# Kernel optimization log

Measured on AMD Instinct MI355X. Metric: run time of the kernel, lower is better.

Reference implementation:

```python
import jax, jax.numpy as jnp
import numpy as np

RADIUS = 0.2
K = 32
H_RES = 480
W_RES = 640
DIM = 128
EPS = 1e-5  # BatchNorm2d default eps


def setup_inputs() -> dict:
    key = jax.random.key(0)
    k1, k2, k3 = jax.random.split(key, 3)
    B, N = 2, 4096
    xyzp = jax.random.normal(k1, (B, N, 4), jnp.float32)
    features = jax.random.normal(k2, (B, N, DIM), jnp.float32)
    Wm = jax.random.normal(k3, (2 * DIM + 9, DIM), jnp.float32) * 0.05
    b = jnp.zeros((DIM,), jnp.float32)
    gamma = jnp.ones((DIM,), jnp.float32)
    beta = jnp.zeros((DIM,), jnp.float32)
    return {"xyzp": xyzp, "features": features, "Wm": Wm, "b": b, "gamma": gamma, "beta": beta}


def _ball_query(xyz, radius, k):
    # pytorch3d-style ball query: first k point indices (in index order) within radius, pad -1
    B, N, _ = xyz.shape
    d2 = jnp.sum((xyz[:, :, None, :] - xyz[:, None, :, :]) ** 2, axis=-1)  # [B,N,N]
    mask = d2 < radius * radius
    keyv = jnp.where(mask, jnp.arange(N)[None, None, :], N)
    order = jnp.argsort(keyv, axis=-1)[:, :, :k]  # stable sort -> first indices within radius
    count = mask.sum(axis=-1)
    return jnp.where(jnp.arange(k)[None, None, :] < count[:, :, None], order, -1)


def _knn_gather(x, idx):
    # x: [B,N,C], idx: [B,N,K] -> [B,N,K,C]
    B, N, Kk = idx.shape
    flat = idx.reshape(B, N * Kk)
    return jnp.take_along_axis(x, flat[:, :, None], axis=1).reshape(B, N, Kk, x.shape[-1])


def reference(xyzp, features, Wm, b, gamma, beta):
    B, N, _ = xyzp.shape
    # detached xyz with z (time) zeroed, used only for neighbor search
    xyz = jax.lax.stop_gradient(xyzp[..., :3]).at[..., 2].set(0.0)
    idx = _ball_query(xyz, RADIUS, K)
    self_idx = jnp.broadcast_to(jnp.arange(N)[None, :, None], (B, N, K))
    idx = jnp.where(idx == -1, self_idx, idx)

    d = xyzp[:, :, None, :] - _knn_gather(xyzp, idx)  # [B,N,K,4]
    ts = d[..., 2:3]
    ts = jnp.where(ts == 0, jnp.float32(1e-6), ts)
    res = jnp.array([W_RES, H_RES], jnp.float32)
    speed = d[..., :2] / ts * res  # [B,N,K,2]
    mean_speed = jnp.broadcast_to(speed.mean(axis=(1, 2), keepdims=True), speed.shape)
    p = jnp.abs(d[..., 3:4])

    knn_f = _knn_gather(features, idx)  # [B,N,K,DIM]
    f0 = jnp.broadcast_to(features[:, :, None, :], (B, N, K, features.shape[-1]))
    f = jnp.concatenate([f0, knn_f, d, speed, p, mean_speed], axis=-1)  # [B,N,K,2*DIM+9]

    h = f @ Wm + b  # Linear
    # BatchNorm2d in training mode: per-channel stats over (B,N,K)
    mu = h.mean(axis=(0, 1, 2))
    var = h.var(axis=(0, 1, 2))
    h = (h - mu) / jnp.sqrt(var + EPS) * gamma + beta
    h = jax.nn.relu(h)
    return h.max(axis=-2)  # max over K neighbors -> [B,N,DIM]
```

## Files before the change

### kernel.cpp

```cpp
#include <hip/hip_runtime.h>
#include <math.h>

#define NB   2
#define NP   4096
#define KNN  32
#define DIMC 128
#define NROWS (NB*NP)
#define MTOT  (NB*NP*KNN)
#define K2BLOCKS 512
#define MAINBLOCKS 512

static constexpr float R2 = 0.04f;

__global__ __launch_bounds__(256) void k1(const float* __restrict__ feat,
                                          const float* __restrict__ Wm,
                                          float* __restrict__ e,
                                          float* __restrict__ g)
{
    const int t    = threadIdx.x;
    const int lane = t & 63;
    const int wid  = __builtin_amdgcn_readfirstlane(t >> 6);
    const int wgl  = blockIdx.x * 4 + wid;
    const int row0 = (wgl >> 2) * 8;
    const int cg   = wgl & 3;
    const int wbase = (cg >> 1) * 128;
    const int c0    = (cg & 1) * 64;

    const float* __restrict__ fptr = feat + (size_t)row0 * DIMC;
    const float* __restrict__ wptr = Wm + (size_t)wbase * DIMC + c0 + lane;

    float acc[8];
    #pragma unroll
    for (int r = 0; r < 8; ++r) acc[r] = 0.f;

    #pragma unroll 2
    for (int k4 = 0; k4 < 32; ++k4) {
        float bv[4];
        #pragma unroll
        for (int j = 0; j < 4; ++j)
            bv[j] = wptr[(size_t)(k4*4 + j)*DIMC];
        float4 as[8];
        #pragma unroll
        for (int r = 0; r < 8; ++r)
            as[r] = *(const float4*)(fptr + (size_t)r*DIMC + k4*4);
        #pragma unroll
        for (int r = 0; r < 8; ++r) {
            acc[r] = fmaf(as[r].x, bv[0], acc[r]);
            acc[r] = fmaf(as[r].y, bv[1], acc[r]);
            acc[r] = fmaf(as[r].z, bv[2], acc[r]);
            acc[r] = fmaf(as[r].w, bv[3], acc[r]);
        }
    }

    float* dst = (cg >> 1) ? g : e;
    #pragma unroll
    for (int r = 0; r < 8; ++r)
        dst[(size_t)(row0 + r)*DIMC + c0 + lane] = acc[r];
}

__global__ __launch_bounds__(256) void k2(const float* __restrict__ xyzp,
                                          const float* __restrict__ e,
                                          const float* __restrict__ g,
                                          const float* __restrict__ Wm,
                                          const float* __restrict__ bbias,
                                          double* __restrict__ spart,
                                          float* __restrict__ hmaxA,
                                          float* __restrict__ hminA,
                                          float* __restrict__ stpartT)
{
    __shared__ float xy[NP*2];
    __shared__ int   idxrow[16*KNN];
    __shared__ float geo[4][2][KNN][8];
    __shared__ float l1s[8][DIMC];
    __shared__ float l2s[8][DIMC];
    __shared__ float swr[8];

    const int bx  = blockIdx.x;
    const int xcd = bx & 7;
    const int pb  = ((xcd >> 2) << 8) + (bx >> 3)*4 + (xcd & 3);
    const int b   = pb >> 8;
    const int p0  = (pb & 255) * 16;

    const int t    = threadIdx.x;
    const int w    = t >> 6;
    const int lane = t & 63;
    const float* xb = xyzp + (size_t)b*NP*4;

    for (int q = t; q < NP; q += 256) {
        const float4 v = *(const float4*)(xb + (size_t)q*4);
        xy[q*2 + 0] = v.x;
        xy[q*2 + 1] = v.y;
    }
    __syncthreads();

    const int pl0 = p0 + w*4;
    unsigned long long wacc[4] = {0ULL, 0ULL, 0ULL, 0ULL};
    {
#pragma clang fp contract(off)
        float xi[4], yi[4];
        #pragma unroll
        for (int p = 0; p < 4; ++p) { xi[p] = xy[(pl0+p)*2]; yi[p] = xy[(pl0+p)*2+1]; }
        for (int c = 0; c < NP/64; ++c) {
            const float2 q = *(const float2*)(xy + (size_t)(c*64 + lane)*2);
            const bool keep = (lane == c);
            #pragma unroll
            for (int p = 0; p < 4; ++p) {
                const float dx = xi[p] - q.x;
                const float dy = yi[p] - q.y;
                const float dx2 = dx*dx;
                const float dy2 = dy*dy;
                const unsigned long long m = __ballot((dx2 + dy2) < R2);
                if (keep) wacc[p] = m;
            }
        }
    }

    #pragma unroll
    for (int p = 0; p < 4; ++p) {
        unsigned long long wd = wacc[p];
        const int cnt = __popcll(wd);
        int pre = cnt;
        #pragma unroll
        for (int off = 1; off < 64; off <<= 1) {
            const int tv = __shfl_up(pre, off);
            if (lane >= off) pre += tv;
        }
        const int total = __shfl(pre, 63);
        int slot = pre - cnt;
        unsigned long long ww = wd;
        while (ww != 0ULL && slot < KNN) {
            const int bpos = __builtin_ctzll(ww);
            idxrow[(w*4 + p)*KNN + slot] = lane*64 + bpos;
            ww &= ww - 1ULL;
            ++slot;
        }
        const int iself = pl0 + p;
        for (int kk = min(total, KNN) + lane; kk < KNN; kk += 64)
            idxrow[(w*4 + p)*KNN + kk] = iself;
    }

    const int half = lane >> 5;
    const int lq   = lane & 31;
    const int c0   = lq * 4;
    float4 w2r[7];
    #pragma unroll
    for (int r = 0; r < 7; ++r)
        w2r[r] = *(const float4*)(Wm + (size_t)(256 + r)*DIMC + c0);
    const float4 bb4 = *(const float4*)(bbias + c0);

    float s1x=0.f,s1y=0.f,s1z=0.f,s1w=0.f;
    float s2x=0.f,s2y=0.f,s2z=0.f,s2w=0.f;
    float sxacc = 0.f, syacc = 0.f;
    const float* gbb = g + (size_t)b*NP*DIMC + c0;

    for (int rp = 0; rp < 2; ++rp) {
        const int rloc = w*4 + rp*2 + half;
        const int ptl  = p0 + rloc;
        const int j0   = idxrow[rloc*KNN + lq];
        const float4 pj = *(const float4*)(xb + (size_t)j0*4);
        const float4 pi = *(const float4*)(xb + (size_t)ptl*4);
        const float dx = pi.x - pj.x;
        const float dy = pi.y - pj.y;
        const float dz = pi.z - pj.z;
        const float dwv = pi.w - pj.w;
        const float ts  = (dz == 0.f) ? 1e-6f : dz;
        const float rts = __builtin_amdgcn_rcpf(ts);
        const float sxv = dx*rts*640.f;
        const float syv = dy*rts*480.f;
        *(float4*)&geo[w][half][lq][0] = make_float4(dx, dy, dz, dwv);
        *(float4*)&geo[w][half][lq][4] = make_float4(sxv, syv, fabsf(dwv), __int_as_float(j0));
        sxacc += sxv; syacc += syv;
        __builtin_amdgcn_wave_barrier();

        const size_t rowg = (size_t)b*NP + ptl;
        const float4 ee = *(const float4*)(e + rowg*DIMC + c0);
        const float ecx = ee.x + bb4.x, ecy = ee.y + bb4.y;
        const float ecz = ee.z + bb4.z, ecw = ee.w + bb4.w;
        float mxx=-INFINITY,mxy=-INFINITY,mxz=-INFINITY,mxw=-INFINITY;
        float mnx= INFINITY,mny= INFINITY,mnz= INFINITY,mnw= INFINITY;
        #pragma unroll 4
        for (int k = 0; k < KNN; ++k) {
            const float4 g0 = *(const float4*)&geo[w][half][k][0];
            const float4 g1 = *(const float4*)&geo[w][half][k][4];
            const int jj = __float_as_int(g1.w);
            const float4 gg = *(const float4*)(gbb + (size_t)jj*DIMC);

            float h0 = ecx + gg.x;
            h0 = fmaf(g0.x, w2r[0].x, h0); h0 = fmaf(g0.y, w2r[1].x, h0);
            h0 = fmaf(g0.z, w2r[2].x, h0); h0 = fmaf(g0.w, w2r[3].x, h0);
            h0 = fmaf(g1.x, w2r[4].x, h0); h0 = fmaf(g1.y, w2r[5].x, h0);
            h0 = fmaf(g1.z, w2r[6].x, h0);
            mxx = fmaxf(mxx, h0); mnx = fminf(mnx, h0);
            s1x += h0; s2x = fmaf(h0, h0, s2x);

            float h1 = ecy + gg.y;
            h1 = fmaf(g0.x, w2r[0].y, h1); h1 = fmaf(g0.y, w2r[1].y, h1);
            h1 = fmaf(g0.z, w2r[2].y, h1); h1 = fmaf(g0.w, w2r[3].y, h1);
            h1 = fmaf(g1.x, w2r[4].y, h1); h1 = fmaf(g1.y, w2r[5].y, h1);
            h1 = fmaf(g1.z, w2r[6].y, h1);
            mxy = fmaxf(mxy, h1); mny = fminf(mny, h1);
            s1y += h1; s2y = fmaf(h1, h1, s2y);

            float h2 = ecz + gg.z;
            h2 = fmaf(g0.x, w2r[0].z, h2); h2 = fmaf(g0.y, w2r[1].z, h2);
            h2 = fmaf(g0.z, w2r[2].z, h2); h2 = fmaf(g0.w, w2r[3].z, h2);
            h2 = fmaf(g1.x, w2r[4].z, h2); h2 = fmaf(g1.y, w2r[5].z, h2);
            h2 = fmaf(g1.z, w2r[6].z, h2);
            mxz = fmaxf(mxz, h2); mnz = fminf(mnz, h2);
            s1z += h2; s2z = fmaf(h2, h2, s2z);

            float h3 = ecw + gg.w;
            h3 = fmaf(g0.x, w2r[0].w, h3); h3 = fmaf(g0.y, w2r[1].w, h3);
            h3 = fmaf(g0.z, w2r[2].w, h3); h3 = fmaf(g0.w, w2r[3].w, h3);
            h3 = fmaf(g1.x, w2r[4].w, h3); h3 = fmaf(g1.y, w2r[5].w, h3);
            h3 = fmaf(g1.z, w2r[6].w, h3);
            mxw = fmaxf(mxw, h3); mnw = fminf(mnw, h3);
            s1w += h3; s2w = fmaf(h3, h3, s2w);
        }
        *(float4*)(hmaxA + rowg*DIMC + c0) = make_float4(mxx, mxy, mxz, mxw);
        *(float4*)(hminA + rowg*DIMC + c0) = make_float4(mnx, mny, mnz, mnw);
        __builtin_amdgcn_wave_barrier();
    }

    #pragma unroll
    for (int off = 32; off > 0; off >>= 1) {
        sxacc += __shfl_down(sxacc, off);
        syacc += __shfl_down(syacc, off);
    }
    if (lane == 0) { swr[w*2] = sxacc; swr[w*2+1] = syacc; }

    *(float4*)&l1s[w*2 + half][c0] = make_float4(s1x, s1y, s1z, s1w);
    *(float4*)&l2s[w*2 + half][c0] = make_float4(s2x, s2y, s2z, s2w);
    __syncthreads();
    if (t < DIMC) {
        float v = 0.f;
        #pragma unroll
        for (int r = 0; r < 8; ++r) v += l1s[r][t];
        stpartT[(size_t)t*MAINBLOCKS + pb] = v;
    } else {
        const int c = t - DIMC;
        float v = 0.f;
        #pragma unroll
        for (int r = 0; r < 8; ++r) v += l2s[r][c];
        stpartT[(size_t)(DIMC + c)*MAINBLOCKS + pb] = v;
    }
    if (t == 0) {
        const double s0 = ((double)swr[0] + (double)swr[2]) + ((double)swr[4] + (double)swr[6]);
        const double s1 = ((double)swr[1] + (double)swr[3]) + ((double)swr[5] + (double)swr[7]);
        spart[(size_t)pb*2 + 0] = s0;
        spart[(size_t)pb*2 + 1] = s1;
    }
}

__global__ __launch_bounds__(256) void kE(const float* __restrict__ stpartT,
                                          const double* __restrict__ spart,
                                          const float* __restrict__ Wm,
                                          const float* __restrict__ gamma,
                                          const float* __restrict__ beta,
                                          float* __restrict__ abuf,
                                          float* __restrict__ dbuf2)
{
    __shared__ double red[256][8];
    const int c = blockIdx.x;
    const int t = threadIdx.x;

    red[t][0] = spart[(size_t)t*2];
    red[t][1] = spart[(size_t)t*2 + 1];
    red[t][2] = spart[(size_t)(t+256)*2];
    red[t][3] = spart[(size_t)(t+256)*2 + 1];
    red[t][4] = (double)stpartT[(size_t)c*MAINBLOCKS + t];
    red[t][5] = (double)stpartT[(size_t)c*MAINBLOCKS + 256 + t];
    red[t][6] = (double)stpartT[(size_t)(c + DIMC)*MAINBLOCKS + t];
    red[t][7] = (double)stpartT[(size_t)(c + DIMC)*MAINBLOCKS + 256 + t];
    __syncthreads();
    for (int st = 128; st > 0; st >>= 1) {
        if (t < st) {
            #pragma unroll
            for (int q = 0; q < 8; ++q) red[t][q] += red[t+st][q];
        }
        __syncthreads();
    }
    if (t == 0) {
        const double NKd = (double)(NP*KNN);
        const float ms0x = (float)(red[0][0] / NKd);
        const float ms0y = (float)(red[0][1] / NKd);
        const float ms1x = (float)(red[0][2] / NKd);
        const float ms1y = (float)(red[0][3] / NKd);
        const float wx = Wm[263*DIMC + c];
        const float wy = Wm[264*DIMC + c];
        const double cb0 = (double)fmaf(ms0x, wx, ms0y*wy);
        const double cb1 = (double)fmaf(ms1x, wx, ms1y*wy);
        const double s1b0 = red[0][4], s1b1 = red[0][5];
        const double s2b0 = red[0][6], s2b1 = red[0][7];
        const double M  = (double)MTOT;
        const double S1 = s1b0 + s1b1 + NKd*(cb0 + cb1);
        const double S2 = (s2b0 + 2.0*cb0*s1b0 + NKd*cb0*cb0)
                        + (s2b1 + 2.0*cb1*s1b1 + NKd*cb1*cb1);
        const double mu  = S1 / M;
        const double var = S2 / M - mu*mu;
        const double inv = 1.0 / sqrt(var + 1e-5);
        const double a  = (double)gamma[c] * inv;
        const double db = (double)beta[c] - mu*a;
        abuf[c] = (float)a;
        dbuf2[c]        = (float)(db + cb0*a);
        dbuf2[DIMC + c] = (float)(db + cb1*a);
    }
}

__global__ __launch_bounds__(256) void kF(const float* __restrict__ hmaxA,
                                          const float* __restrict__ hminA,
                                          const float* __restrict__ abuf,
                                          const float* __restrict__ dbuf2,
                                          float* __restrict__ out)
{
    const int gid = blockIdx.x*256 + threadIdx.x;
    const int row = gid >> 6;
    const int c0  = (gid & 63)*2;
    const int b   = row >> 12;
    const size_t off = (size_t)row*DIMC + c0;
    const float2 mx = *(const float2*)(hmaxA + off);
    const float2 mn = *(const float2*)(hminA + off);
    const float a0 = abuf[c0],  a1 = abuf[c0+1];
    const float d0 = dbuf2[b*DIMC + c0], d1 = dbuf2[b*DIMC + c0 + 1];
    const float h0 = (a0 >= 0.f) ? mx.x : mn.x;
    const float h1 = (a1 >= 0.f) ? mx.y : mn.y;
    float2 o;
    o.x = fmaxf(fmaf(h0, a0, d0), 0.0f);
    o.y = fmaxf(fmaf(h1, a1, d1), 0.0f);
    *(float2*)(out + off) = o;
}

extern "C" void kernel_launch(void* const* d_in, const int* in_sizes, int n_in,
                              void* d_out, int out_size, void* d_ws, size_t ws_size,
                              hipStream_t stream)
{
    const float* xyzp  = (const float*)d_in[0];
    const float* feat  = (const float*)d_in[1];
    const float* Wm    = (const float*)d_in[2];
    const float* bbias = (const float*)d_in[3];
    const float* gamma = (const float*)d_in[4];
    const float* beta  = (const float*)d_in[5];

    char* ws = (char*)d_ws;
    const size_t MB = 1u << 20;
    float*  g       = (float*) (ws + 1*MB);
    float*  e       = (float*) (ws + 5*MB);
    float*  hmaxA   = (float*) (ws + 9*MB);
    float*  hminA   = (float*) (ws + 13*MB);
    double* spart   = (double*)(ws + 17*MB);
    float*  abuf    = (float*) (ws + 17*MB + 65536);
    float*  dbuf2   = (float*) (ws + 17*MB + 66560);
    float*  stpartT = (float*) (ws + 18*MB);

    k1 <<<1024, 256, 0, stream>>>(feat, Wm, e, g);
    k2 <<<K2BLOCKS, 256, 0, stream>>>(xyzp, e, g, Wm, bbias, spart, hmaxA, hminA, stpartT);
    kE <<<DIMC, 256, 0, stream>>>(stpartT, spart, Wm, gamma, beta, abuf, dbuf2);
    kF <<<(NROWS*64)/256, 256, 0, stream>>>(hmaxA, hminA, abuf, dbuf2, (float*)d_out);
}
```

Before: 53.30 us.

## Compute feature projection GEMM with bf16 MFMA after a prepack conversion kernel

Replaces the scalar FP32 FMA GEMM that projects features through the first two Wm blocks with a bf16 MFMA 16x16x32 kernel. A new pre-kernel converts the features and weights to bf16 and packs them into the MFMA operand layout. This targets the arithmetic cost of the small GEMM, but it adds an extra launch and a conversion pass, and the bf16 rounding lowers precision of e and g.

```diff
diff --git a/kernel.cpp b/kernel.cpp
--- a/kernel.cpp
+++ b/kernel.cpp
@@ -12,50 +12,87 @@
 
 static constexpr float R2 = 0.04f;
 
-__global__ __launch_bounds__(256) void k1(const float* __restrict__ feat,
+typedef short bf16x8 __attribute__((ext_vector_type(8)));
+typedef float f32x4  __attribute__((ext_vector_type(4)));
+
+__device__ __forceinline__ unsigned short f2bf(float f) {
+    unsigned u = __float_as_uint(f);
+    return (unsigned short)((u + 0x7FFFu + ((u >> 16) & 1u)) >> 16);
+}
+
+__global__ __launch_bounds__(256) void kC(const float* __restrict__ feat,
                                           const float* __restrict__ Wm,
-                                          float* __restrict__ e,
-                                          float* __restrict__ g)
+                                          uint4* __restrict__ featb,
+                                          uint4* __restrict__ Wb)
+{
+    const int bx = blockIdx.x;
+    if (bx < 512) {
+        const int s  = bx*256 + threadIdx.x;
+        const int l  = s & 63;
+        const int ks = (s >> 6) & 3;
+        const int rt = s >> 8;
+        const int row = rt*16 + (l & 15);
+        const int kb  = ks*32 + ((l >> 4) << 3);
+        const float4 v0 = *(const float4*)(feat + (size_t)row*DIMC + kb);
+        const float4 v1 = *(const float4*)(feat + (size_t)row*DIMC + kb + 4);
+        uint4 o;
+        o.x = (unsigned)f2bf(v0.x) | ((unsigned)f2bf(v0.y) << 16);
+        o.y = (unsigned)f2bf(v0.z) | ((unsigned)f2bf(v0.w) << 16);
+        o.z = (unsigned)f2bf(v1.x) | ((unsigned)f2bf(v1.y) << 16);
+        o.w = (unsigned)f2bf(v1.z) | ((unsigned)f2bf(v1.w) << 16);
+        featb[s] = o;
+    } else {
+        const int s2 = (bx - 512)*256 + threadIdx.x;
+        const int l  = s2 & 63;
+        const int ks = (s2 >> 6) & 3;
+        const int ct = s2 >> 8;
+        const int c  = ct*16 + (l & 15);
+        const int kb = ks*32 + ((l >> 4) << 3);
+        const float* src = Wm + (size_t)((c >> 7)*128 + kb)*DIMC + (c & 127);
+        unsigned short b[8];
+        #pragma unroll
+        for (int j = 0; j < 8; ++j) b[j] = f2bf(src[(size_t)j*DIMC]);
+        uint4 o;
+        o.x = (unsigned)b[0] | ((unsigned)b[1] << 16);
+        o.y = (unsigned)b[2] | ((unsigned)b[3] << 16);
+        o.z = (unsigned)b[4] | ((unsigned)b[5] << 16);
+        o.w = (unsigned)b[6] | ((unsigned)b[7] << 16);
+        Wb[s2] = o;
+    }
+}
+
+__global__ __launch_bounds__(256) void k1m(const bf16x8* __restrict__ featb,
+                                           const bf16x8* __restrict__ Wb,
+                                           float* __restrict__ e,
+                                           float* __restrict__ g)
 {
     const int t    = threadIdx.x;
+    const int w    = t >> 6;
     const int lane = t & 63;
-    const int wid  = __builtin_amdgcn_readfirstlane(t >> 6);
-    const int wgl  = blockIdx.x * 4 + wid;
-    const int row0 = (wgl >> 2) * 8;
-    const int cg   = wgl & 3;
-    const int wbase = (cg >> 1) * 128;
-    const int c0    = (cg & 1) * 64;
-
-    const float* __restrict__ fptr = feat + (size_t)row0 * DIMC;
-    const float* __restrict__ wptr = Wm + (size_t)wbase * DIMC + c0 + lane;
-
-    float acc[8];
-    #pragma unroll
-    for (int r = 0; r < 8; ++r) acc[r] = 0.f;
-
-    #pragma unroll 2
-    for (int k4 = 0; k4 < 32; ++k4) {
-        float bv[4];
-        #pragma unroll
-        for (int j = 0; j < 4; ++j)
-            bv[j] = wptr[(size_t)(k4*4 + j)*DIMC];
-        float4 as[8];
-        #pragma unroll
-        for (int r = 0; r < 8; ++r)
-            as[r] = *(const float4*)(fptr + (size_t)r*DIMC + k4*4);
-        #pragma unroll
-        for (int r = 0; r < 8; ++r) {
-            acc[r] = fmaf(as[r].x, bv[0], acc[r]);
-            acc[r] = fmaf(as[r].y, bv[1], acc[r]);
-            acc[r] = fmaf(as[r].z, bv[2], acc[r]);
-            acc[r] = fmaf(as[r].w, bv[3], acc[r]);
-        }
-    }
-
-    float* dst = (cg >> 1) ? g : e;
-    #pragma unroll
-    for (int r = 0; r < 8; ++r)
-        dst[(size_t)(row0 + r)*DIMC + c0 + lane] = acc[r];
+    const int rt   = blockIdx.x;
+
+    bf16x8 af[4];
+    #pragma unroll
+    for (int ks = 0; ks < 4; ++ks)
+        af[ks] = featb[(size_t)(rt*4 + ks)*64 + lane];
+
+    #pragma unroll
+    for (int ct = 0; ct < 4; ++ct) {
+        const int ctg = w*4 + ct;
+        f32x4 acc = {0.f, 0.f, 0.f, 0.f};
+        #pragma unroll
+        for (int ks = 0; ks < 4; ++ks) {
+            const bf16x8 bb = Wb[(size_t)(ctg*4 + ks)*64 + lane];
+            acc = __builtin_amdgcn_mfma_f32_16x16x32_bf16(af[ks], bb, acc, 0, 0, 0);
+        }
+        const int cg = ctg*16 + (lane & 15);
+        float* dst = (cg < 128) ? e : g;
+        const int cc = cg & 127;
+        const int r0 = (lane >> 4) * 4;
+        #pragma unroll
+        for (int r = 0; r < 4; ++r)
+            dst[(size_t)(rt*16 + r0 + r)*DIMC + cc] = acc[r];
+    }
 }
 
 __global__ __launch_bounds__(256) void k2(const float* __restrict__ xyzp,
@@ -351,9 +388,12 @@
     float*  abuf    = (float*) (ws + 17*MB + 65536);
     float*  dbuf2   = (float*) (ws + 17*MB + 66560);
     float*  stpartT = (float*) (ws + 18*MB);
-
-    k1 <<<1024, 256, 0, stream>>>(feat, Wm, e, g);
-    k2 <<<K2BLOCKS, 256, 0, stream>>>(xyzp, e, g, Wm, bbias, spart, hmaxA, hminA, stpartT);
-    kE <<<DIMC, 256, 0, stream>>>(stpartT, spart, Wm, gamma, beta, abuf, dbuf2);
-    kF <<<(NROWS*64)/256, 256, 0, stream>>>(hmaxA, hminA, abuf, dbuf2, (float*)d_out);
-}
+    uint4*  featb   = (uint4*) (ws + 19*MB);
+    uint4*  Wb      = (uint4*) (ws + 21*MB);
+
+    kC  <<<528, 256, 0, stream>>>(feat, Wm, featb, Wb);
+    k1m <<<512, 256, 0, stream>>>((const bf16x8*)featb, (const bf16x8*)Wb, e, g);
+    k2  <<<K2BLOCKS, 256, 0, stream>>>(xyzp, e, g, Wm, bbias, spart, hmaxA, hminA, stpartT);
+    kE  <<<DIMC, 256, 0, stream>>>(stpartT, spart, Wm, gamma, beta, abuf, dbuf2);
+    kF  <<<(NROWS*64)/256, 256, 0, stream>>>(hmaxA, hminA, abuf, dbuf2, (float*)d_out);
+}
```

New measurement: 50.10 us. 6.0% less time.

## Use bf16 MFMA for feature projection and store max/min in bf16

Applied to the files above, without the earlier changes.

Replaces the scalar FP32 projection of features onto the two weight halves with bf16 MFMA 16x16x32 instructions, converting inputs to bf16 in registers. Also packs the per-row max and min intermediates into bf16 pairs in one uint4 buffer, which halves that traffic, and vectorizes the final epilogue to float4. The aim is to cut compute in the first GEMM and memory traffic between the main and final kernels, at the cost of bf16 rounding error in the projections and the pooled values.

```diff
diff --git a/kernel.cpp b/kernel.cpp
--- a/kernel.cpp
+++ b/kernel.cpp
@@ -12,50 +12,67 @@
 
 static constexpr float R2 = 0.04f;
 
-__global__ __launch_bounds__(256) void k1(const float* __restrict__ feat,
-                                          const float* __restrict__ Wm,
-                                          float* __restrict__ e,
-                                          float* __restrict__ g)
+typedef short bf16x8 __attribute__((ext_vector_type(8)));
+typedef float f32x4  __attribute__((ext_vector_type(4)));
+
+__device__ __forceinline__ unsigned f2bf(float f) {
+    unsigned u = __float_as_uint(f);
+    return ((u + 0x7FFFu + ((u >> 16) & 1u)) >> 16);
+}
+__device__ __forceinline__ float bf2f(unsigned us) {
+    return __uint_as_float(us << 16);
+}
+__device__ __forceinline__ bf16x8 pack8(float4 v0, float4 v1) {
+    union { unsigned u[4]; bf16x8 b; } o;
+    o.u[0] = f2bf(v0.x) | (f2bf(v0.y) << 16);
+    o.u[1] = f2bf(v0.z) | (f2bf(v0.w) << 16);
+    o.u[2] = f2bf(v1.x) | (f2bf(v1.y) << 16);
+    o.u[3] = f2bf(v1.z) | (f2bf(v1.w) << 16);
+    return o.b;
+}
+
+__global__ __launch_bounds__(256) void k1m(const float* __restrict__ feat,
+                                           const float* __restrict__ Wm,
+                                           float* __restrict__ e,
+                                           float* __restrict__ g)
 {
     const int t    = threadIdx.x;
+    const int w    = t >> 6;
     const int lane = t & 63;
-    const int wid  = __builtin_amdgcn_readfirstlane(t >> 6);
-    const int wgl  = blockIdx.x * 4 + wid;
-    const int row0 = (wgl >> 2) * 8;
-    const int cg   = wgl & 3;
-    const int wbase = (cg >> 1) * 128;
-    const int c0    = (cg & 1) * 64;
-
-    const float* __restrict__ fptr = feat + (size_t)row0 * DIMC;
-    const float* __restrict__ wptr = Wm + (size_t)wbase * DIMC + c0 + lane;
-
-    float acc[8];
-    #pragma unroll
-    for (int r = 0; r < 8; ++r) acc[r] = 0.f;
-
-    #pragma unroll 2
-    for (int k4 = 0; k4 < 32; ++k4) {
-        float bv[4];
-        #pragma unroll
-        for (int j = 0; j < 4; ++j)
-            bv[j] = wptr[(size_t)(k4*4 + j)*DIMC];
-        float4 as[8];
-        #pragma unroll
-        for (int r = 0; r < 8; ++r)
-            as[r] = *(const float4*)(fptr + (size_t)r*DIMC + k4*4);
-        #pragma unroll
-        for (int r = 0; r < 8; ++r) {
-            acc[r] = fmaf(as[r].x, bv[0], acc[r]);
-            acc[r] = fmaf(as[r].y, bv[1], acc[r]);
-            acc[r] = fmaf(as[r].z, bv[2], acc[r]);
-            acc[r] = fmaf(as[r].w, bv[3], acc[r]);
-        }
-    }
-
-    float* dst = (cg >> 1) ? g : e;
-    #pragma unroll
-    for (int r = 0; r < 8; ++r)
-        dst[(size_t)(row0 + r)*DIMC + c0 + lane] = acc[r];
+    const int rt   = blockIdx.x;
+    const int r    = lane & 15;
+    const int kg   = lane >> 4;
+
+    bf16x8 af[4];
+    const float* arow = feat + (size_t)(rt*16 + r)*DIMC + kg*8;
+    #pragma unroll
+    for (int ks = 0; ks < 4; ++ks) {
+        const float4 v0 = *(const float4*)(arow + ks*32);
+        const float4 v1 = *(const float4*)(arow + ks*32 + 4);
+        af[ks] = pack8(v0, v1);
+    }
+
+    const float* wcol = Wm + (size_t)(w >> 1)*128*DIMC + (w & 1)*64 + r;
+    float* dst = (w >> 1) ? g : e;
+    const int ccb = (w & 1)*64 + r;
+
+    #pragma unroll
+    for (int ct = 0; ct < 4; ++ct) {
+        f32x4 acc = {0.f, 0.f, 0.f, 0.f};
+        #pragma unroll
+        for (int ks = 0; ks < 4; ++ks) {
+            const float* bsrc = wcol + (size_t)(ks*32 + kg*8)*DIMC + ct*16;
+            float bv[8];
+            #pragma unroll
+            for (int j = 0; j < 8; ++j) bv[j] = bsrc[(size_t)j*DIMC];
+            const bf16x8 bb = pack8(make_float4(bv[0],bv[1],bv[2],bv[3]),
+                                    make_float4(bv[4],bv[5],bv[6],bv[7]));
+            acc = __builtin_amdgcn_mfma_f32_16x16x32_bf16(af[ks], bb, acc, 0, 0, 0);
+        }
+        #pragma unroll
+        for (int reg = 0; reg < 4; ++reg)
+            dst[(size_t)(rt*16 + kg*4 + reg)*DIMC + ccb + ct*16] = acc[reg];
+    }
 }
 
 __global__ __launch_bounds__(256) void k2(const float* __restrict__ xyzp,
@@ -64,8 +81,7 @@
                                           const float* __restrict__ Wm,
                                           const float* __restrict__ bbias,
                                           double* __restrict__ spart,
-                                          float* __restrict__ hmaxA,
-                                          float* __restrict__ hminA,
+                                          uint4* __restrict__ hmm,
                                           float* __restrict__ stpartT)
 {
     __shared__ float xy[NP*2];
@@ -217,8 +233,12 @@
             mxw = fmaxf(mxw, h3); mnw = fminf(mnw, h3);
             s1w += h3; s2w = fmaf(h3, h3, s2w);
         }
-        *(float4*)(hmaxA + rowg*DIMC + c0) = make_float4(mxx, mxy, mxz, mxw);
-        *(float4*)(hminA + rowg*DIMC + c0) = make_float4(mnx, mny, mnz, mnw);
+        uint4 o;
+        o.x = f2bf(mxx) | (f2bf(mxy) << 16);
+        o.y = f2bf(mxz) | (f2bf(mxw) << 16);
+        o.z = f2bf(mnx) | (f2bf(mny) << 16);
+        o.w = f2bf(mnz) | (f2bf(mnw) << 16);
+        hmm[rowg*32 + lq] = o;
         __builtin_amdgcn_wave_barrier();
     }
 
@@ -307,27 +327,29 @@
     }
 }
 
-__global__ __launch_bounds__(256) void kF(const float* __restrict__ hmaxA,
-                                          const float* __restrict__ hminA,
+__global__ __launch_bounds__(256) void kF(const uint4* __restrict__ hmm,
                                           const float* __restrict__ abuf,
                                           const float* __restrict__ dbuf2,
                                           float* __restrict__ out)
 {
     const int gid = blockIdx.x*256 + threadIdx.x;
-    const int row = gid >> 6;
-    const int c0  = (gid & 63)*2;
+    const int row = gid >> 5;
+    const int lq  = gid & 31;
+    const int c0  = lq * 4;
     const int b   = row >> 12;
-    const size_t off = (size_t)row*DIMC + c0;
-    const float2 mx = *(const float2*)(hmaxA + off);
-    const float2 mn = *(const float2*)(hminA + off);
-    const float a0 = abuf[c0],  a1 = abuf[c0+1];
-    const float d0 = dbuf2[b*DIMC + c0], d1 = dbuf2[b*DIMC + c0 + 1];
-    const float h0 = (a0 >= 0.f) ? mx.x : mn.x;
-    const float h1 = (a1 >= 0.f) ? mx.y : mn.y;
-    float2 o;
-    o.x = fmaxf(fmaf(h0, a0, d0), 0.0f);
-    o.y = fmaxf(fmaf(h1, a1, d1), 0.0f);
-    *(float2*)(out + off) = o;
+    const uint4 p = hmm[(size_t)row*32 + lq];
+    const float4 a4 = *(const float4*)(abuf + c0);
+    const float4 d4 = *(const float4*)(dbuf2 + b*DIMC + c0);
+    const float mx0 = bf2f(p.x & 0xFFFFu), mx1 = bf2f(p.x >> 16);
+    const float mx2 = bf2f(p.y & 0xFFFFu), mx3 = bf2f(p.y >> 16);
+    const float mn0 = bf2f(p.z & 0xFFFFu), mn1 = bf2f(p.z >> 16);
+    const float mn2 = bf2f(p.w & 0xFFFFu), mn3 = bf2f(p.w >> 16);
+    float4 o;
+    o.x = fmaxf(fmaf((a4.x >= 0.f) ? mx0 : mn0, a4.x, d4.x), 0.f);
+    o.y = fmaxf(fmaf((a4.y >= 0.f) ? mx1 : mn1, a4.y, d4.y), 0.f);
+    o.z = fmaxf(fmaf((a4.z >= 0.f) ? mx2 : mn2, a4.z, d4.z), 0.f);
+    o.w = fmaxf(fmaf((a4.w >= 0.f) ? mx3 : mn3, a4.w, d4.w), 0.f);
+    *(float4*)(out + (size_t)row*DIMC + c0) = o;
 }
 
 extern "C" void kernel_launch(void* const* d_in, const int* in_sizes, int n_in,
@@ -345,15 +367,14 @@
     const size_t MB = 1u << 20;
     float*  g       = (float*) (ws + 1*MB);
     float*  e       = (float*) (ws + 5*MB);
-    float*  hmaxA   = (float*) (ws + 9*MB);
-    float*  hminA   = (float*) (ws + 13*MB);
+    uint4*  hmm     = (uint4*) (ws + 9*MB);
     double* spart   = (double*)(ws + 17*MB);
     float*  abuf    = (float*) (ws + 17*MB + 65536);
     float*  dbuf2   = (float*) (ws + 17*MB + 66560);
     float*  stpartT = (float*) (ws + 18*MB);
 
-    k1 <<<1024, 256, 0, stream>>>(feat, Wm, e, g);
-    k2 <<<K2BLOCKS, 256, 0, stream>>>(xyzp, e, g, Wm, bbias, spart, hmaxA, hminA, stpartT);
-    kE <<<DIMC, 256, 0, stream>>>(stpartT, spart, Wm, gamma, beta, abuf, dbuf2);
-    kF <<<(NROWS*64)/256, 256, 0, stream>>>(hmaxA, hminA, abuf, dbuf2, (float*)d_out);
-}
+    k1m <<<512, 256, 0, stream>>>(feat, Wm, e, g);
+    k2  <<<K2BLOCKS, 256, 0, stream>>>(xyzp, e, g, Wm, bbias, spart, hmm, stpartT);
+    kE  <<<DIMC, 256, 0, stream>>>(stpartT, spart, Wm, gamma, beta, abuf, dbuf2);
+    kF  <<<(NROWS*32)/256, 256, 0, stream>>>(hmm, abuf, dbuf2, (float*)d_out);
+}
```

Result: faster. 47.94 us (-10.1%).
